# Kernel optimization log

Measured on AMD Instinct MI355X. Metric: run time of the kernel, lower is better.

The kernel has to match this reference:

```python
import jax, jax.numpy as jnp
import numpy as np

B, I, L = 128, 32, 96   # batch, input_dim, time_series_length
H = 512                  # hidden_dim
F = 24                   # forecast_length (t_eval points)
S = 16                   # n_samples


def _lin(k, out_dim, in_dim):
    kw, kb = jax.random.split(k)
    bound = 1.0 / np.sqrt(in_dim)
    W = jax.random.uniform(kw, (out_dim, in_dim), jnp.float32, -bound, bound)
    b = jax.random.uniform(kb, (out_dim,), jnp.float32, -bound, bound)
    return W, b


def setup_inputs() -> dict:
    key = jax.random.key(0)
    ks = jax.random.split(key, 12)
    enc_Wih, enc_bih = _lin(ks[0], 3 * H, I)
    enc_Whh, enc_bhh = _lin(ks[1], 3 * H, H)
    f_W1, f_b1 = _lin(ks[2], H, H)
    f_W2, f_b2 = _lin(ks[3], H, H)
    g_W, g_b = _lin(ks[4], H, H)
    dec_Wih, dec_bih = _lin(ks[5], 3 * H, H)
    dec_Whh, dec_bhh = _lin(ks[6], 3 * H, H)
    out_W, out_b = _lin(ks[7], I, H)
    x = jax.random.normal(ks[8], (B, I, L), jnp.float32)
    noise = jax.random.normal(ks[9], (S, F - 1, B, H), jnp.float32)  # unit normals -> dW = sqrt(dt)*noise
    return dict(x=x, noise=noise,
                enc_Wih=enc_Wih, enc_Whh=enc_Whh, enc_bih=enc_bih, enc_bhh=enc_bhh,
                f_W1=f_W1, f_b1=f_b1, f_W2=f_W2, f_b2=f_b2,
                g_W=g_W, g_b=g_b,
                dec_Wih=dec_Wih, dec_Whh=dec_Whh, dec_bih=dec_bih, dec_bhh=dec_bhh,
                out_W=out_W, out_b=out_b)


def _gru_cell(gi, gh, h):
    ir, iz, inn = jnp.split(gi, 3, axis=-1)
    hr, hz, hn = jnp.split(gh, 3, axis=-1)
    r = jax.nn.sigmoid(ir + hr)
    z = jax.nn.sigmoid(iz + hz)
    n = jnp.tanh(inn + r * hn)
    return (1.0 - z) * n + z * h


def reference(x, noise, enc_Wih, enc_Whh, enc_bih, enc_bhh,
              f_W1, f_b1, f_W2, f_b2, g_W, g_b,
              dec_Wih, dec_Whh, dec_bih, dec_bhh, out_W, out_b):
    Bb, Ii = x.shape[0], x.shape[1]
    Ss, steps = noise.shape[0], noise.shape[1]
    Hh = enc_Whh.shape[1]
    Ff = steps + 1  # forecast_length; t_eval=linspace(0,F,F) -> F-1 euler steps

    # ---- encoder GRU over [B, L, I] (x permuted from [B, I, L]) ----
    xs = jnp.transpose(x, (0, 2, 1))  # [B, L, I]
    gi_all = jnp.einsum('bli,gi->lbg', xs, enc_Wih) + enc_bih  # [L, B, 3H]

    def enc_step(h, gi):
        gh = h @ enc_Whh.T + enc_bhh
        return _gru_cell(gi, gh, h), None

    h0 = jnp.zeros((Bb, Hh), x.dtype)
    h_enc, _ = jax.lax.scan(enc_step, h0, gi_all)  # [B, H]

    # ---- Euler-Maruyama SDE integration, samples merged into batch ----
    dt = Ff / steps  # linspace(0, F, F): dt = F/(F-1)
    sqdt = jnp.sqrt(jnp.asarray(dt, x.dtype))
    h_sde = jnp.broadcast_to(h_enc, (Ss, Bb, Hh)).reshape(Ss * Bb, Hh)
    dW = (noise * sqdt).transpose(1, 0, 2, 3).reshape(steps, Ss * Bb, Hh)

    def sde_step(h, dw):
        f = jnp.tanh(h @ f_W1.T + f_b1) @ f_W2.T + f_b2
        g = jax.nn.softplus(h @ g_W.T + g_b)
        return h + f * dt + g * dw, None

    h_T, _ = jax.lax.scan(sde_step, h_sde, dW)  # [S*B, H]

    # ---- decoder GRU with zero inputs (input proj reduces to bias) ----
    gi0 = dec_bih  # W_ih @ 0 + b_ih

    def dec_step(h, _):
        gh = h @ dec_Whh.T + dec_bhh
        h_new = _gru_cell(gi0, gh, h)
        return h_new, h_new

    _, hs = jax.lax.scan(dec_step, h_T, None, length=Ff)  # [F, S*B, H]

    out = hs @ out_W.T + out_b          # [F, S*B, I]
    out = out.transpose(1, 2, 0)        # [S*B, I, F]
    return out.reshape(Ss, Bb, Ii, Ff)  # [S, B, I, F]
```

## Files before the change

### kernel.cpp

```cpp
#include <hip/hip_runtime.h>
#include <math.h>

typedef __bf16 bf16x8 __attribute__((ext_vector_type(8)));
typedef float f32x4 __attribute__((ext_vector_type(4)));
typedef unsigned long long u64;

#define HD 512
#define NB 128
#define NI 32
#define NL 96
#define NS 16
#define NF 24
#define NSTEP 23
#define PAD 520

#define MFMA16(a,b,c) __builtin_amdgcn_mfma_f32_16x16x32_bf16(a,b,c,0,0,0)

__device__ __forceinline__ unsigned short f2bf(float f) {
    union { float f; unsigned u; } v; v.f = f;
    unsigned r = v.u + 0x7fffu + ((v.u >> 16) & 1u);
    return (unsigned short)(r >> 16);
}
__device__ __forceinline__ float bf2f(unsigned short h) {
    union { unsigned u; float f; } v; v.u = ((unsigned)h) << 16;
    return v.f;
}
__device__ __forceinline__ void split_bf(float v, unsigned short& hi, unsigned short& lo) {
    unsigned short h = f2bf(v);
    hi = h;
    lo = f2bf(v - bf2f(h));
}
__device__ __forceinline__ float sigm(float x) { return 1.0f / (1.0f + __expf(-x)); }
__device__ __forceinline__ float softp(float x) {
    return fmaxf(x, 0.0f) + log1pf(__expf(-fabsf(x)));
}
__device__ __forceinline__ bf16x8 ld8(const unsigned short* p) {
    return *reinterpret_cast<const bf16x8*>(p);
}
__device__ __forceinline__ f32x4 mfma3(bf16x8 ahi, bf16x8 alo, const unsigned short* bp, f32x4 c) {
    bf16x8 bhi = ld8(bp);
    bf16x8 blo = ld8(bp + 8);
    c = MFMA16(ahi, bhi, c);
    c = MFMA16(alo, bhi, c);
    c = MFMA16(ahi, blo, c);
    return c;
}

__global__ void pack_w(const float* __restrict__ W, unsigned short* __restrict__ Wp,
                       int N, int K) {
    int idx = blockIdx.x * 256 + threadIdx.x;
    int total = (N / 16) * (K / 32) * 64;
    if (idx >= total) return;
    int lane = idx & 63;
    int t2 = idx >> 6;
    int KT = K / 32;
    int kt = t2 % KT, nt = t2 / KT;
    const float* src = W + (size_t)(nt * 16 + (lane & 15)) * K + kt * 32 + (lane >> 4) * 8;
    unsigned short* dst = Wp + (size_t)idx * 16;
    #pragma unroll
    for (int j = 0; j < 8; ++j) split_bf(src[j], dst[j], dst[8 + j]);
}

__global__ void pack_x(const float* __restrict__ x, unsigned short* __restrict__ xhi,
                       unsigned short* __restrict__ xlo) {
    int idx = blockIdx.x * 256 + threadIdx.x;
    if (idx >= NL * NB) return;
    int b = idx % NB, l = idx / NB;
    size_t base = (size_t)(l * NB + b) * NI;
    #pragma unroll
    for (int i = 0; i < NI; ++i)
        split_bf(x[((size_t)b * NI + i) * NL + l], xhi[base + i], xlo[base + i]);
}

__global__ __launch_bounds__(512, 2) void coop_all(
    const unsigned short* __restrict__ xhi, const unsigned short* __restrict__ xlo,
    const unsigned short* __restrict__ wih_p, const unsigned short* __restrict__ whh_p,
    const unsigned short* __restrict__ w1_p, const unsigned short* __restrict__ w2_p,
    const unsigned short* __restrict__ gw_p, const unsigned short* __restrict__ dwhh_p,
    const unsigned short* __restrict__ outw_p,
    const float* __restrict__ ebih, const float* __restrict__ ebhh,
    const float* __restrict__ fb1, const float* __restrict__ fb2,
    const float* __restrict__ gb, const float* __restrict__ dbih,
    const float* __restrict__ dbhh, const float* __restrict__ outb,
    const float* __restrict__ noise,
    u64* hS0h, u64* hS0l, u64* hS1h, u64* hS1l,
    float* out, unsigned* bar)
{
    const int bid = blockIdx.x;
    const int tid = threadIdx.x, lane = tid & 63, wv = tid >> 6;
    const int l15 = lane & 15, g4 = lane >> 4;
    const f32x4 zz = {0.f, 0.f, 0.f, 0.f};

    __shared__ float pred[4][8][16][16];
    __shared__ __align__(16) unsigned short hAhi[16][PAD];
    __shared__ __align__(16) unsigned short hAlo[16][PAD];
    __shared__ __align__(16) unsigned short uAhi[16][PAD];
    __shared__ __align__(16) unsigned short uAlo[16][PAD];
    __shared__ __align__(16) unsigned short Shi[16][16], Slo[16][16];

    u64* bufh[2] = {hS0h, hS1h};
    u64* bufl[2] = {hS0l, hS1l};

    {
        const int m = bid >> 5, n = bid & 31;
        unsigned* fl = bar + m * 32;
        float cr = 0.f, cz = 0.f, binx = 0.f, bhnn = 0.f, hcell = 0.f;
        const int crow = tid >> 4, cunit = tid & 15;
        if (tid < 256) {
            int u = n * 16 + cunit;
            cr = ebih[u] + ebhh[u];
            cz = ebih[HD + u] + ebhh[HD + u];
            binx = ebih[2 * HD + u];
            bhnn = ebhh[2 * HD + u];
        }
        #pragma unroll 1
        for (int l = 0; l < NL; ++l) {
            bf16x8 axh, axl;
            if (wv == 0) {
                size_t xb = ((size_t)l * NB + m * 16 + l15) * NI + g4 * 8;
                axh = ld8(xhi + xb);
                axl = ld8(xlo + xb);
            }
            if (l > 0) {
                if (wv == 0) {
                    for (;;) {
                        unsigned v = __hip_atomic_load(fl + (lane & 31),
                                     __ATOMIC_RELAXED, __HIP_MEMORY_SCOPE_AGENT);
                        if (__all((int)(v >= (unsigned)l))) break;
                        __builtin_amdgcn_s_sleep(2);
                    }
                }
                __syncthreads();
            }
            {
                const u64* sh = bufh[l & 1];
                const u64* sl = bufl[l & 1];
                u64 qh[4], ql[4];
                #pragma unroll
                for (int rep = 0; rep < 4; ++rep) {
                    int idx = rep * 512 + tid;
                    int r = idx >> 7, c4 = idx & 127;
                    qh[rep] = __hip_atomic_load(sh + (size_t)(m * 16 + r) * 128 + c4,
                                                __ATOMIC_RELAXED, __HIP_MEMORY_SCOPE_AGENT);
                    ql[rep] = __hip_atomic_load(sl + (size_t)(m * 16 + r) * 128 + c4,
                                                __ATOMIC_RELAXED, __HIP_MEMORY_SCOPE_AGENT);
                }
                #pragma unroll
                for (int rep = 0; rep < 4; ++rep) {
                    int idx = rep * 512 + tid;
                    int r = idx >> 7, c4 = idx & 127;
                    *(u64*)&hAhi[r][c4 * 4] = qh[rep];
                    *(u64*)&hAlo[r][c4 * 4] = ql[rep];
                }
            }
            __syncthreads();
            f32x4 pr = zz, pz = zz, pnh = zz, pnx = zz;
            if (wv == 0) {
                pr  = mfma3(axh, axl, wih_p + ((size_t)(0 * 32 + n) * 64 + lane) * 16, pr);
                pz  = mfma3(axh, axl, wih_p + ((size_t)(1 * 32 + n) * 64 + lane) * 16, pz);
                pnx = mfma3(axh, axl, wih_p + ((size_t)(2 * 32 + n) * 64 + lane) * 16, pnx);
            }
            #pragma unroll
            for (int kk = 0; kk < 2; ++kk) {
                int kt = wv * 2 + kk;
                bf16x8 ah = *(const bf16x8*)&hAhi[l15][kt * 32 + g4 * 8];
                bf16x8 al = *(const bf16x8*)&hAlo[l15][kt * 32 + g4 * 8];
                pr  = mfma3(ah, al, whh_p + ((size_t)((0 * 32 + n) * 16 + kt) * 64 + lane) * 16, pr);
                pz  = mfma3(ah, al, whh_p + ((size_t)((1 * 32 + n) * 16 + kt) * 64 + lane) * 16, pz);
                pnh = mfma3(ah, al, whh_p + ((size_t)((2 * 32 + n) * 16 + kt) * 64 + lane) * 16, pnh);
            }
            #pragma unroll
            for (int v = 0; v < 4; ++v) {
                pred[0][wv][g4 * 4 + v][l15] = pr[v];
                pred[1][wv][g4 * 4 + v][l15] = pz[v];
                pred[2][wv][g4 * 4 + v][l15] = pnh[v];
                if (wv == 0) pred[3][0][g4 * 4 + v][l15] = pnx[v];
            }
            __syncthreads();
            if (tid < 256) {
                float ar = 0.f, az = 0.f, anh_ = 0.f;
                #pragma unroll
                for (int w = 0; w < 8; ++w) {
                    ar += pred[0][w][crow][cunit];
                    az += pred[1][w][crow][cunit];
                    anh_ += pred[2][w][crow][cunit];
                }
                float anx_ = pred[3][0][crow][cunit];
                float r = sigm(ar + cr);
                float z = sigm(az + cz);
                float nn = tanhf(anx_ + binx + r * (anh_ + bhnn));
                hcell = (1.f - z) * nn + z * hcell;
                unsigned short hi, lo;
                split_bf(hcell, hi, lo);
                Shi[crow][cunit] = hi;
                Slo[crow][cunit] = lo;
            }
            __syncthreads();
            if (tid < 128) {
                int p = tid >> 6, t = tid & 63;
                int r = t >> 2, c4 = t & 3;
                u64 q = p ? *(const u64*)&Slo[r][c4 * 4] : *(const u64*)&Shi[r][c4 * 4];
                u64* dst = p ? bufl[(l + 1) & 1] : bufh[(l + 1) & 1];
                __hip_atomic_store(dst + (size_t)(m * 16 + r) * 128 + n * 4 + c4, q,
                                   __ATOMIC_RELAXED, __HIP_MEMORY_SCOPE_AGENT);
            }
            __builtin_amdgcn_s_waitcnt(0);
            __syncthreads();
            if (tid == 0)
                __hip_atomic_store(fl + n, (unsigned)(l + 1),
                                   __ATOMIC_RELAXED, __HIP_MEMORY_SCOPE_AGENT);
        }
        if (tid == 0)
            __hip_atomic_fetch_add(bar + 256, 1u, __ATOMIC_RELAXED, __HIP_MEMORY_SCOPE_AGENT);
    }

    if (bid >= 128) return;

    if (tid == 0) {
        while (__hip_atomic_load(bar + 256, __ATOMIC_RELAXED, __HIP_MEMORY_SCOPE_AGENT) < 256u)
            __builtin_amdgcn_s_sleep(2);
    }
    __syncthreads();

    const int s = bid >> 3, t7 = bid & 7;
    const int brow = t7 * 16;

    for (int i = tid; i < 2048; i += 512) {
        int r = i >> 7, c4 = i & 127;
        u64 qh = __hip_atomic_load(hS0h + (size_t)(brow + r) * 128 + c4, __ATOMIC_RELAXED, __HIP_MEMORY_SCOPE_AGENT);
        u64 ql = __hip_atomic_load(hS0l + (size_t)(brow + r) * 128 + c4, __ATOMIC_RELAXED, __HIP_MEMORY_SCOPE_AGENT);
        *(u64*)&hAhi[r][c4 * 4] = qh;
        *(u64*)&hAlo[r][c4 * 4] = ql;
    }
    __syncthreads();

    float hreg[4][4];
    #pragma unroll
    for (int nt = 0; nt < 4; ++nt)
        #pragma unroll
        for (int v = 0; v < 4; ++v) {
            int u = wv * 64 + nt * 16 + l15;
            hreg[nt][v] = bf2f(hAhi[g4 * 4 + v][u]) + bf2f(hAlo[g4 * 4 + v][u]);
        }

    float b1v[4], b2v[4], gbv[4];
    #pragma unroll
    for (int nt = 0; nt < 4; ++nt) {
        int u = wv * 64 + nt * 16 + l15;
        b1v[nt] = fb1[u]; b2v[nt] = fb2[u]; gbv[nt] = gb[u];
    }
    const float dt = (float)NF / (float)NSTEP;
    const float sqdt = sqrtf(dt);

    #pragma unroll 1
    for (int st = 0; st < NSTEP; ++st) {
        f32x4 au[4], ag[4];
        #pragma unroll
        for (int nt = 0; nt < 4; ++nt) { au[nt] = zz; ag[nt] = zz; }
        #pragma unroll 2
        for (int kt = 0; kt < 16; ++kt) {
            bf16x8 ah = *(const bf16x8*)&hAhi[l15][kt * 32 + g4 * 8];
            bf16x8 al = *(const bf16x8*)&hAlo[l15][kt * 32 + g4 * 8];
            #pragma unroll
            for (int nt = 0; nt < 4; ++nt) {
                int un = wv * 4 + nt;
                au[nt] = mfma3(ah, al, w1_p + ((size_t)(un * 16 + kt) * 64 + lane) * 16, au[nt]);
                ag[nt] = mfma3(ah, al, gw_p + ((size_t)(un * 16 + kt) * 64 + lane) * 16, ag[nt]);
            }
        }
        float nz[4][4];
        #pragma unroll
        for (int nt = 0; nt < 4; ++nt)
            #pragma unroll
            for (int v = 0; v < 4; ++v)
                nz[nt][v] = noise[((size_t)(s * NSTEP + st) * NB + brow + g4 * 4 + v) * HD
                                  + wv * 64 + nt * 16 + l15];
        #pragma unroll
        for (int nt = 0; nt < 4; ++nt)
            #pragma unroll
            for (int v = 0; v < 4; ++v) {
                unsigned short hi, lo;
                split_bf(tanhf(au[nt][v] + b1v[nt]), hi, lo);
                uAhi[g4 * 4 + v][wv * 64 + nt * 16 + l15] = hi;
                uAlo[g4 * 4 + v][wv * 64 + nt * 16 + l15] = lo;
            }
        __syncthreads();
        f32x4 af[4];
        #pragma unroll
        for (int nt = 0; nt < 4; ++nt) af[nt] = zz;
        #pragma unroll 2
        for (int kt = 0; kt < 16; ++kt) {
            bf16x8 uh = *(const bf16x8*)&uAhi[l15][kt * 32 + g4 * 8];
            bf16x8 ul = *(const bf16x8*)&uAlo[l15][kt * 32 + g4 * 8];
            #pragma unroll
            for (int nt = 0; nt < 4; ++nt)
                af[nt] = mfma3(uh, ul, w2_p + ((size_t)((wv * 4 + nt) * 16 + kt) * 64 + lane) * 16, af[nt]);
        }
        #pragma unroll
        for (int nt = 0; nt < 4; ++nt)
            #pragma unroll
            for (int v = 0; v < 4; ++v) {
                float gg = softp(ag[nt][v] + gbv[nt]);
                hreg[nt][v] += (af[nt][v] + b2v[nt]) * dt + gg * sqdt * nz[nt][v];
                unsigned short hi, lo;
                split_bf(hreg[nt][v], hi, lo);
                hAhi[g4 * 4 + v][wv * 64 + nt * 16 + l15] = hi;
                hAlo[g4 * 4 + v][wv * 64 + nt * 16 + l15] = lo;
            }
        __syncthreads();
    }

    float crv[4], czv[4], binv[4], bhnv[4];
    #pragma unroll
    for (int nt = 0; nt < 4; ++nt) {
        int u = wv * 64 + nt * 16 + l15;
        crv[nt] = dbih[u] + dbhh[u];
        czv[nt] = dbih[HD + u] + dbhh[HD + u];
        binv[nt] = dbih[2 * HD + u];
        bhnv[nt] = dbhh[2 * HD + u];
    }
    const float obias = (wv < 2) ? outb[wv * 16 + l15] : 0.f;

    #pragma unroll 1
    for (int j = 0; j <= NF; ++j) {
        if (j >= 1 && wv < 2) {
            f32x4 ao = zz;
            #pragma unroll 2
            for (int kt = 0; kt < 16; ++kt) {
                bf16x8 ah = *(const bf16x8*)&hAhi[l15][kt * 32 + g4 * 8];
                bf16x8 al = *(const bf16x8*)&hAlo[l15][kt * 32 + g4 * 8];
                ao = mfma3(ah, al, outw_p + ((size_t)(wv * 16 + kt) * 64 + lane) * 16, ao);
            }
            #pragma unroll
            for (int v = 0; v < 4; ++v)
                out[(((size_t)s * NB + brow + g4 * 4 + v) * NI + wv * 16 + l15) * NF + (j - 1)]
                    = ao[v] + obias;
        }
        if (j == NF) break;
        f32x4 ar[4], az[4], anh[4];
        #pragma unroll
        for (int nt = 0; nt < 4; ++nt) { ar[nt] = zz; az[nt] = zz; anh[nt] = zz; }
        #pragma unroll 2
        for (int kt = 0; kt < 16; ++kt) {
            bf16x8 ah = *(const bf16x8*)&hAhi[l15][kt * 32 + g4 * 8];
            bf16x8 al = *(const bf16x8*)&hAlo[l15][kt * 32 + g4 * 8];
            #pragma unroll
            for (int nt = 0; nt < 4; ++nt) {
                int un = wv * 4 + nt;
                ar[nt]  = mfma3(ah, al, dwhh_p + ((size_t)((un) * 16 + kt) * 64 + lane) * 16, ar[nt]);
                az[nt]  = mfma3(ah, al, dwhh_p + ((size_t)((32 + un) * 16 + kt) * 64 + lane) * 16, az[nt]);
                anh[nt] = mfma3(ah, al, dwhh_p + ((size_t)((64 + un) * 16 + kt) * 64 + lane) * 16, anh[nt]);
            }
        }
        #pragma unroll
        for (int nt = 0; nt < 4; ++nt)
            #pragma unroll
            for (int v = 0; v < 4; ++v) {
                float r = sigm(ar[nt][v] + crv[nt]);
                float z = sigm(az[nt][v] + czv[nt]);
                float nn2 = tanhf(binv[nt] + r * (anh[nt][v] + bhnv[nt]));
                hreg[nt][v] = (1.f - z) * nn2 + z * hreg[nt][v];
            }
        __syncthreads();
        #pragma unroll
        for (int nt = 0; nt < 4; ++nt)
            #pragma unroll
            for (int v = 0; v < 4; ++v) {
                unsigned short hi, lo;
                split_bf(hreg[nt][v], hi, lo);
                hAhi[g4 * 4 + v][wv * 64 + nt * 16 + l15] = hi;
                hAlo[g4 * 4 + v][wv * 64 + nt * 16 + l15] = lo;
            }
        __syncthreads();
    }
}

extern "C" void kernel_launch(void* const* d_in, const int* in_sizes, int n_in,
                              void* d_out, int out_size, void* d_ws, size_t ws_size,
                              hipStream_t stream) {
    const float* x       = (const float*)d_in[0];
    const float* noise   = (const float*)d_in[1];
    const float* enc_Wih = (const float*)d_in[2];
    const float* enc_Whh = (const float*)d_in[3];
    const float* enc_bih = (const float*)d_in[4];
    const float* enc_bhh = (const float*)d_in[5];
    const float* f_W1    = (const float*)d_in[6];
    const float* f_b1    = (const float*)d_in[7];
    const float* f_W2    = (const float*)d_in[8];
    const float* f_b2    = (const float*)d_in[9];
    const float* g_W     = (const float*)d_in[10];
    const float* g_b     = (const float*)d_in[11];
    const float* dec_Whh = (const float*)d_in[13];
    const float* dec_bih = (const float*)d_in[14];
    const float* dec_bhh = (const float*)d_in[15];
    const float* out_W   = (const float*)d_in[16];
    const float* out_b   = (const float*)d_in[17];
    float* out = (float*)d_out;

    char* ws = (char*)d_ws;
    unsigned short* whh_p  = (unsigned short*)(ws + 0);
    unsigned short* wih_p  = (unsigned short*)(ws + 3145728);
    unsigned short* w1_p   = (unsigned short*)(ws + 3342336);
    unsigned short* w2_p   = (unsigned short*)(ws + 4390912);
    unsigned short* gw_p   = (unsigned short*)(ws + 5439488);
    unsigned short* dwhh_p = (unsigned short*)(ws + 6488064);
    unsigned short* outw_p = (unsigned short*)(ws + 9633792);
    unsigned short* xhi    = (unsigned short*)(ws + 9699328);
    unsigned short* xlo    = (unsigned short*)(ws + 10485760);
    u64*            hS0h   = (u64*)(ws + 11272192);
    u64*            hS0l   = (u64*)(ws + 11403264);
    u64*            hS1h   = (u64*)(ws + 11534336);
    u64*            hS1l   = (u64*)(ws + 11665408);
    unsigned*       bar    = (unsigned*)(ws + 11796480);

    hipMemsetAsync(ws + 11272192, 0, 262144, stream);
    hipMemsetAsync(ws + 11796480, 0, 2048, stream);

    pack_w<<<384, 256, 0, stream>>>(enc_Whh, whh_p, 3 * HD, HD);
    pack_w<<<24, 256, 0, stream>>>(enc_Wih, wih_p, 3 * HD, NI);
    pack_w<<<128, 256, 0, stream>>>(f_W1, w1_p, HD, HD);
    pack_w<<<128, 256, 0, stream>>>(f_W2, w2_p, HD, HD);
    pack_w<<<128, 256, 0, stream>>>(g_W, gw_p, HD, HD);
    pack_w<<<384, 256, 0, stream>>>(dec_Whh, dwhh_p, 3 * HD, HD);
    pack_w<<<8, 256, 0, stream>>>(out_W, outw_p, NI, HD);
    pack_x<<<48, 256, 0, stream>>>(x, xhi, xlo);

    void* args[] = {
        (void*)&xhi, (void*)&xlo, (void*)&wih_p, (void*)&whh_p,
        (void*)&w1_p, (void*)&w2_p, (void*)&gw_p, (void*)&dwhh_p, (void*)&outw_p,
        (void*)&enc_bih, (void*)&enc_bhh, (void*)&f_b1, (void*)&f_b2,
        (void*)&g_b, (void*)&dec_bih, (void*)&dec_bhh, (void*)&out_b,
        (void*)&noise,
        (void*)&hS0h, (void*)&hS0l, (void*)&hS1h, (void*)&hS1l,
        (void*)&out, (void*)&bar
    };
    hipLaunchCooperativeKernel((void*)coop_all, dim3(256), dim3(512), args, 0, stream);
}
```

Baseline: 1.982 ms.

## Split SDE and decoder phases across all 256 blocks with group flag sync

Before, only 128 blocks ran the SDE and decoder phases, each owning 16 rows and all 512 hidden units. Now all 256 blocks take part: groups of 8 blocks share 64 rows, and each block computes a 64-unit column slice. Intermediate activations are exchanged through global buffers with per-group flag barriers. This doubles the active compute units and cuts per-block weight traffic, at the cost of two extra global exchange and sync rounds per SDE step and one per decoder step.

```diff
diff --git a/kernel.cpp b/kernel.cpp
--- a/kernel.cpp
+++ b/kernel.cpp
@@ -44,6 +44,58 @@
     c = MFMA16(alo, bhi, c);
     c = MFMA16(ahi, blo, c);
     return c;
+}
+
+__device__ __forceinline__ void sigval(unsigned* slot, unsigned val, int tid) {
+    __builtin_amdgcn_s_waitcnt(0);
+    __syncthreads();
+    if (tid == 0)
+        __hip_atomic_store(slot, val, __ATOMIC_RELAXED, __HIP_MEMORY_SCOPE_AGENT);
+}
+__device__ __forceinline__ void poll8(const unsigned* f, unsigned tgt, int wv, int lane) {
+    if (wv == 0) {
+        for (;;) {
+            unsigned v = __hip_atomic_load(f + (lane & 7), __ATOMIC_RELAXED, __HIP_MEMORY_SCOPE_AGENT);
+            if (__all((int)(v >= tgt))) break;
+            __builtin_amdgcn_s_sleep(2);
+        }
+    }
+    __syncthreads();
+}
+__device__ __forceinline__ void stage64(const u64* sh, const u64* sl, int r0,
+        unsigned short (*Ahi)[16][PAD], unsigned short (*Alo)[16][PAD], int tid) {
+    #pragma unroll 1
+    for (int c = 0; c < 4; ++c) {
+        u64 th[4], tl[4];
+        #pragma unroll
+        for (int k = 0; k < 4; ++k) {
+            int idx = (c * 4 + k) * 512 + tid;
+            int r = idx >> 7, c4 = idx & 127;
+            th[k] = __hip_atomic_load(sh + (size_t)(r0 + r) * 128 + c4,
+                                      __ATOMIC_RELAXED, __HIP_MEMORY_SCOPE_AGENT);
+            tl[k] = __hip_atomic_load(sl + (size_t)(r0 + r) * 128 + c4,
+                                      __ATOMIC_RELAXED, __HIP_MEMORY_SCOPE_AGENT);
+        }
+        #pragma unroll
+        for (int k = 0; k < 4; ++k) {
+            int idx = (c * 4 + k) * 512 + tid;
+            int r = idx >> 7, c4 = idx & 127;
+            *(u64*)&Ahi[r >> 4][r & 15][c4 * 4] = th[k];
+            *(u64*)&Alo[r >> 4][r & 15][c4 * 4] = tl[k];
+        }
+    }
+}
+__device__ __forceinline__ void publish64(u64* dh, u64* dl, int r0, int u0c,
+        unsigned short (*Bhi)[72], unsigned short (*Blo)[72], int tid) {
+    #pragma unroll
+    for (int rep = 0; rep < 4; ++rep) {
+        int idx = rep * 512 + tid;
+        int pl = idx >> 10, e = idx & 1023;
+        int r = e >> 4, c = e & 15;
+        u64 q = pl ? *(const u64*)&Blo[r][c * 4] : *(const u64*)&Bhi[r][c * 4];
+        u64* dst = (pl ? dl : dh) + (size_t)(r0 + r) * 128 + u0c + c;
+        __hip_atomic_store(dst, q, __ATOMIC_RELAXED, __HIP_MEMORY_SCOPE_AGENT);
+    }
 }
 
 __global__ void pack_w(const float* __restrict__ W, unsigned short* __restrict__ Wp,
@@ -84,6 +136,7 @@
     const float* __restrict__ dbhh, const float* __restrict__ outb,
     const float* __restrict__ noise,
     u64* hS0h, u64* hS0l, u64* hS1h, u64* hS1l,
+    u64* uPh, u64* uPl, u64* hD0h, u64* hD0l, u64* hD1h, u64* hD1l,
     float* out, unsigned* bar)
 {
     const int bid = blockIdx.x;
@@ -91,12 +144,16 @@
     const int l15 = lane & 15, g4 = lane >> 4;
     const f32x4 zz = {0.f, 0.f, 0.f, 0.f};
 
-    __shared__ float pred[4][8][16][16];
-    __shared__ __align__(16) unsigned short hAhi[16][PAD];
-    __shared__ __align__(16) unsigned short hAlo[16][PAD];
-    __shared__ __align__(16) unsigned short uAhi[16][PAD];
-    __shared__ __align__(16) unsigned short uAlo[16][PAD];
-    __shared__ __align__(16) unsigned short Shi[16][16], Slo[16][16];
+    __shared__ __align__(16) unsigned char SM[151552];
+    auto hA64hi = reinterpret_cast<unsigned short (*)[16][PAD]>(SM);
+    auto hA64lo = reinterpret_cast<unsigned short (*)[16][PAD]>(SM + 66560);
+    auto uShi   = reinterpret_cast<unsigned short (*)[72]>(SM + 133120);
+    auto uSlo   = reinterpret_cast<unsigned short (*)[72]>(SM + 142336);
+    auto pred   = reinterpret_cast<float (*)[8][16][16]>(SM);
+    auto ehAhi  = reinterpret_cast<unsigned short (*)[PAD]>(SM + 32768);
+    auto ehAlo  = reinterpret_cast<unsigned short (*)[PAD]>(SM + 49408);
+    auto Shi    = reinterpret_cast<unsigned short (*)[16]>(SM + 66048);
+    auto Slo    = reinterpret_cast<unsigned short (*)[16]>(SM + 66560);
 
     u64* bufh[2] = {hS0h, hS1h};
     u64* bufl[2] = {hS0l, hS1l};
@@ -149,8 +206,8 @@
                 for (int rep = 0; rep < 4; ++rep) {
                     int idx = rep * 512 + tid;
                     int r = idx >> 7, c4 = idx & 127;
-                    *(u64*)&hAhi[r][c4 * 4] = qh[rep];
-                    *(u64*)&hAlo[r][c4 * 4] = ql[rep];
+                    *(u64*)&ehAhi[r][c4 * 4] = qh[rep];
+                    *(u64*)&ehAlo[r][c4 * 4] = ql[rep];
                 }
             }
             __syncthreads();
@@ -163,8 +220,8 @@
             #pragma unroll
             for (int kk = 0; kk < 2; ++kk) {
                 int kt = wv * 2 + kk;
-                bf16x8 ah = *(const bf16x8*)&hAhi[l15][kt * 32 + g4 * 8];
-                bf16x8 al = *(const bf16x8*)&hAlo[l15][kt * 32 + g4 * 8];
+                bf16x8 ah = *(const bf16x8*)&ehAhi[l15][kt * 32 + g4 * 8];
+                bf16x8 al = *(const bf16x8*)&ehAlo[l15][kt * 32 + g4 * 8];
                 pr  = mfma3(ah, al, whh_p + ((size_t)((0 * 32 + n) * 16 + kt) * 64 + lane) * 16, pr);
                 pz  = mfma3(ah, al, whh_p + ((size_t)((1 * 32 + n) * 16 + kt) * 64 + lane) * 16, pz);
                 pnh = mfma3(ah, al, whh_p + ((size_t)((2 * 32 + n) * 16 + kt) * 64 + lane) * 16, pnh);
@@ -214,39 +271,38 @@
             __hip_atomic_fetch_add(bar + 256, 1u, __ATOMIC_RELAXED, __HIP_MEMORY_SCOPE_AGENT);
     }
 
-    if (bid >= 128) return;
-
     if (tid == 0) {
         while (__hip_atomic_load(bar + 256, __ATOMIC_RELAXED, __HIP_MEMORY_SCOPE_AGENT) < 256u)
             __builtin_amdgcn_s_sleep(2);
     }
     __syncthreads();
 
-    const int s = bid >> 3, t7 = bid & 7;
-    const int brow = t7 * 16;
-
-    for (int i = tid; i < 2048; i += 512) {
-        int r = i >> 7, c4 = i & 127;
-        u64 qh = __hip_atomic_load(hS0h + (size_t)(brow + r) * 128 + c4, __ATOMIC_RELAXED, __HIP_MEMORY_SCOPE_AGENT);
-        u64 ql = __hip_atomic_load(hS0l + (size_t)(brow + r) * 128 + c4, __ATOMIC_RELAXED, __HIP_MEMORY_SCOPE_AGENT);
-        *(u64*)&hAhi[r][c4 * 4] = qh;
-        *(u64*)&hAlo[r][c4 * 4] = ql;
-    }
+    const int m2 = bid >> 3, n2 = bid & 7;
+    const int rt = wv & 3, nc = wv >> 2;
+    const int r0g = m2 * 64;
+    const int u0 = n2 * 64, u0c = n2 * 16;
+    const int s = m2 >> 1, b0 = (m2 & 1) * 64;
+    unsigned* uf = bar + 320 + m2 * 8;
+    unsigned* hf = bar + 576 + m2 * 8;
+    u64* hDh[2] = {hD0h, hD1h};
+    u64* hDl[2] = {hD0l, hD1l};
+
+    stage64(hS0h, hS0l, b0, hA64hi, hA64lo, tid);
     __syncthreads();
 
-    float hreg[4][4];
+    float hreg[2][4];
     #pragma unroll
-    for (int nt = 0; nt < 4; ++nt)
+    for (int nt = 0; nt < 2; ++nt)
         #pragma unroll
         for (int v = 0; v < 4; ++v) {
-            int u = wv * 64 + nt * 16 + l15;
-            hreg[nt][v] = bf2f(hAhi[g4 * 4 + v][u]) + bf2f(hAlo[g4 * 4 + v][u]);
-        }
-
-    float b1v[4], b2v[4], gbv[4];
+            int cc = u0 + nc * 32 + nt * 16 + l15;
+            hreg[nt][v] = bf2f(hA64hi[rt][g4 * 4 + v][cc]) + bf2f(hA64lo[rt][g4 * 4 + v][cc]);
+        }
+
+    float b1v[2], b2v[2], gbv[2];
     #pragma unroll
-    for (int nt = 0; nt < 4; ++nt) {
-        int u = wv * 64 + nt * 16 + l15;
+    for (int nt = 0; nt < 2; ++nt) {
+        int u = u0 + nc * 32 + nt * 16 + l15;
         b1v[nt] = fb1[u]; b2v[nt] = fb2[u]; gbv[nt] = gb[u];
     }
     const float dt = (float)NF / (float)NSTEP;
@@ -254,123 +310,138 @@
 
     #pragma unroll 1
     for (int st = 0; st < NSTEP; ++st) {
-        f32x4 au[4], ag[4];
-        #pragma unroll
-        for (int nt = 0; nt < 4; ++nt) { au[nt] = zz; ag[nt] = zz; }
+        f32x4 au[2] = {zz, zz}, ag[2] = {zz, zz};
         #pragma unroll 2
         for (int kt = 0; kt < 16; ++kt) {
-            bf16x8 ah = *(const bf16x8*)&hAhi[l15][kt * 32 + g4 * 8];
-            bf16x8 al = *(const bf16x8*)&hAlo[l15][kt * 32 + g4 * 8];
-            #pragma unroll
-            for (int nt = 0; nt < 4; ++nt) {
-                int un = wv * 4 + nt;
-                au[nt] = mfma3(ah, al, w1_p + ((size_t)(un * 16 + kt) * 64 + lane) * 16, au[nt]);
-                ag[nt] = mfma3(ah, al, gw_p + ((size_t)(un * 16 + kt) * 64 + lane) * 16, ag[nt]);
-            }
-        }
-        float nz[4][4];
-        #pragma unroll
-        for (int nt = 0; nt < 4; ++nt)
+            bf16x8 ah = *(const bf16x8*)&hA64hi[rt][l15][kt * 32 + g4 * 8];
+            bf16x8 al = *(const bf16x8*)&hA64lo[rt][l15][kt * 32 + g4 * 8];
+            #pragma unroll
+            for (int nt = 0; nt < 2; ++nt) {
+                int ntg = n2 * 4 + nc * 2 + nt;
+                au[nt] = mfma3(ah, al, w1_p + ((size_t)(ntg * 16 + kt) * 64 + lane) * 16, au[nt]);
+                ag[nt] = mfma3(ah, al, gw_p + ((size_t)(ntg * 16 + kt) * 64 + lane) * 16, ag[nt]);
+            }
+        }
+        float nz[2][4];
+        #pragma unroll
+        for (int nt = 0; nt < 2; ++nt)
             #pragma unroll
             for (int v = 0; v < 4; ++v)
-                nz[nt][v] = noise[((size_t)(s * NSTEP + st) * NB + brow + g4 * 4 + v) * HD
-                                  + wv * 64 + nt * 16 + l15];
-        #pragma unroll
-        for (int nt = 0; nt < 4; ++nt)
+                nz[nt][v] = noise[((size_t)(s * NSTEP + st) * NB + b0 + rt * 16 + g4 * 4 + v) * HD
+                                  + u0 + nc * 32 + nt * 16 + l15];
+        #pragma unroll
+        for (int nt = 0; nt < 2; ++nt)
             #pragma unroll
             for (int v = 0; v < 4; ++v) {
                 unsigned short hi, lo;
                 split_bf(tanhf(au[nt][v] + b1v[nt]), hi, lo);
-                uAhi[g4 * 4 + v][wv * 64 + nt * 16 + l15] = hi;
-                uAlo[g4 * 4 + v][wv * 64 + nt * 16 + l15] = lo;
+                uShi[rt * 16 + g4 * 4 + v][nc * 32 + nt * 16 + l15] = hi;
+                uSlo[rt * 16 + g4 * 4 + v][nc * 32 + nt * 16 + l15] = lo;
             }
         __syncthreads();
-        f32x4 af[4];
-        #pragma unroll
-        for (int nt = 0; nt < 4; ++nt) af[nt] = zz;
+        publish64(uPh, uPl, r0g, u0c, uShi, uSlo, tid);
+        sigval(uf + n2, (unsigned)(st + 1), tid);
+        poll8(uf, (unsigned)(st + 1), wv, lane);
+        stage64(uPh, uPl, r0g, hA64hi, hA64lo, tid);
+        __syncthreads();
+        f32x4 af[2] = {zz, zz};
         #pragma unroll 2
         for (int kt = 0; kt < 16; ++kt) {
-            bf16x8 uh = *(const bf16x8*)&uAhi[l15][kt * 32 + g4 * 8];
-            bf16x8 ul = *(const bf16x8*)&uAlo[l15][kt * 32 + g4 * 8];
-            #pragma unroll
-            for (int nt = 0; nt < 4; ++nt)
-                af[nt] = mfma3(uh, ul, w2_p + ((size_t)((wv * 4 + nt) * 16 + kt) * 64 + lane) * 16, af[nt]);
-        }
-        #pragma unroll
-        for (int nt = 0; nt < 4; ++nt)
+            bf16x8 uh = *(const bf16x8*)&hA64hi[rt][l15][kt * 32 + g4 * 8];
+            bf16x8 ul = *(const bf16x8*)&hA64lo[rt][l15][kt * 32 + g4 * 8];
+            #pragma unroll
+            for (int nt = 0; nt < 2; ++nt) {
+                int ntg = n2 * 4 + nc * 2 + nt;
+                af[nt] = mfma3(uh, ul, w2_p + ((size_t)(ntg * 16 + kt) * 64 + lane) * 16, af[nt]);
+            }
+        }
+        #pragma unroll
+        for (int nt = 0; nt < 2; ++nt)
             #pragma unroll
             for (int v = 0; v < 4; ++v) {
                 float gg = softp(ag[nt][v] + gbv[nt]);
                 hreg[nt][v] += (af[nt][v] + b2v[nt]) * dt + gg * sqdt * nz[nt][v];
                 unsigned short hi, lo;
                 split_bf(hreg[nt][v], hi, lo);
-                hAhi[g4 * 4 + v][wv * 64 + nt * 16 + l15] = hi;
-                hAlo[g4 * 4 + v][wv * 64 + nt * 16 + l15] = lo;
+                uShi[rt * 16 + g4 * 4 + v][nc * 32 + nt * 16 + l15] = hi;
+                uSlo[rt * 16 + g4 * 4 + v][nc * 32 + nt * 16 + l15] = lo;
             }
         __syncthreads();
-    }
-
-    float crv[4], czv[4], binv[4], bhnv[4];
+        publish64(hDh[(st + 1) & 1], hDl[(st + 1) & 1], r0g, u0c, uShi, uSlo, tid);
+        sigval(hf + n2, (unsigned)(st + 1), tid);
+        poll8(hf, (unsigned)(st + 1), wv, lane);
+        stage64(hDh[(st + 1) & 1], hDl[(st + 1) & 1], r0g, hA64hi, hA64lo, tid);
+        __syncthreads();
+    }
+
+    float crv[2], czv[2], binv[2], bhnv[2];
     #pragma unroll
-    for (int nt = 0; nt < 4; ++nt) {
-        int u = wv * 64 + nt * 16 + l15;
+    for (int nt = 0; nt < 2; ++nt) {
+        int u = u0 + nc * 32 + nt * 16 + l15;
         crv[nt] = dbih[u] + dbhh[u];
         czv[nt] = dbih[HD + u] + dbhh[HD + u];
         binv[nt] = dbih[2 * HD + u];
         bhnv[nt] = dbhh[2 * HD + u];
     }
-    const float obias = (wv < 2) ? outb[wv * 16 + l15] : 0.f;
+    float obias[2] = {0.f, 0.f};
+    if (n2 == 0 && wv < 4) {
+        obias[0] = outb[l15];
+        obias[1] = outb[16 + l15];
+    }
 
     #pragma unroll 1
     for (int j = 0; j <= NF; ++j) {
-        if (j >= 1 && wv < 2) {
-            f32x4 ao = zz;
+        if (j >= 1 && n2 == 0 && wv < 4) {
+            f32x4 ao[2] = {zz, zz};
             #pragma unroll 2
             for (int kt = 0; kt < 16; ++kt) {
-                bf16x8 ah = *(const bf16x8*)&hAhi[l15][kt * 32 + g4 * 8];
-                bf16x8 al = *(const bf16x8*)&hAlo[l15][kt * 32 + g4 * 8];
-                ao = mfma3(ah, al, outw_p + ((size_t)(wv * 16 + kt) * 64 + lane) * 16, ao);
-            }
-            #pragma unroll
-            for (int v = 0; v < 4; ++v)
-                out[(((size_t)s * NB + brow + g4 * 4 + v) * NI + wv * 16 + l15) * NF + (j - 1)]
-                    = ao[v] + obias;
+                bf16x8 ah = *(const bf16x8*)&hA64hi[rt][l15][kt * 32 + g4 * 8];
+                bf16x8 al = *(const bf16x8*)&hA64lo[rt][l15][kt * 32 + g4 * 8];
+                #pragma unroll
+                for (int nt = 0; nt < 2; ++nt)
+                    ao[nt] = mfma3(ah, al, outw_p + ((size_t)(nt * 16 + kt) * 64 + lane) * 16, ao[nt]);
+            }
+            #pragma unroll
+            for (int nt = 0; nt < 2; ++nt)
+                #pragma unroll
+                for (int v = 0; v < 4; ++v) {
+                    int b = b0 + rt * 16 + g4 * 4 + v;
+                    out[(((size_t)s * NB + b) * NI + nt * 16 + l15) * NF + (j - 1)]
+                        = ao[nt][v] + obias[nt];
+                }
         }
         if (j == NF) break;
-        f32x4 ar[4], az[4], anh[4];
-        #pragma unroll
-        for (int nt = 0; nt < 4; ++nt) { ar[nt] = zz; az[nt] = zz; anh[nt] = zz; }
+        f32x4 ar[2] = {zz, zz}, az[2] = {zz, zz}, anh[2] = {zz, zz};
         #pragma unroll 2
         for (int kt = 0; kt < 16; ++kt) {
-            bf16x8 ah = *(const bf16x8*)&hAhi[l15][kt * 32 + g4 * 8];
-            bf16x8 al = *(const bf16x8*)&hAlo[l15][kt * 32 + g4 * 8];
-            #pragma unroll
-            for (int nt = 0; nt < 4; ++nt) {
-                int un = wv * 4 + nt;
-                ar[nt]  = mfma3(ah, al, dwhh_p + ((size_t)((un) * 16 + kt) * 64 + lane) * 16, ar[nt]);
-                az[nt]  = mfma3(ah, al, dwhh_p + ((size_t)((32 + un) * 16 + kt) * 64 + lane) * 16, az[nt]);
-                anh[nt] = mfma3(ah, al, dwhh_p + ((size_t)((64 + un) * 16 + kt) * 64 + lane) * 16, anh[nt]);
-            }
-        }
-        #pragma unroll
-        for (int nt = 0; nt < 4; ++nt)
+            bf16x8 ah = *(const bf16x8*)&hA64hi[rt][l15][kt * 32 + g4 * 8];
+            bf16x8 al = *(const bf16x8*)&hA64lo[rt][l15][kt * 32 + g4 * 8];
+            #pragma unroll
+            for (int nt = 0; nt < 2; ++nt) {
+                int ntg = n2 * 4 + nc * 2 + nt;
+                ar[nt]  = mfma3(ah, al, dwhh_p + ((size_t)((ntg) * 16 + kt) * 64 + lane) * 16, ar[nt]);
+                az[nt]  = mfma3(ah, al, dwhh_p + ((size_t)((32 + ntg) * 16 + kt) * 64 + lane) * 16, az[nt]);
+                anh[nt] = mfma3(ah, al, dwhh_p + ((size_t)((64 + ntg) * 16 + kt) * 64 + lane) * 16, anh[nt]);
+            }
+        }
+        #pragma unroll
+        for (int nt = 0; nt < 2; ++nt)
             #pragma unroll
             for (int v = 0; v < 4; ++v) {
                 float r = sigm(ar[nt][v] + crv[nt]);
                 float z = sigm(az[nt][v] + czv[nt]);
                 float nn2 = tanhf(binv[nt] + r * (anh[nt][v] + bhnv[nt]));
                 hreg[nt][v] = (1.f - z) * nn2 + z * hreg[nt][v];
-            }
-        __syncthreads();
-        #pragma unroll
-        for (int nt = 0; nt < 4; ++nt)
-            #pragma unroll
-            for (int v = 0; v < 4; ++v) {
                 unsigned short hi, lo;
                 split_bf(hreg[nt][v], hi, lo);
-                hAhi[g4 * 4 + v][wv * 64 + nt * 16 + l15] = hi;
-                hAlo[g4 * 4 + v][wv * 64 + nt * 16 + l15] = lo;
-            }
+                uShi[rt * 16 + g4 * 4 + v][nc * 32 + nt * 16 + l15] = hi;
+                uSlo[rt * 16 + g4 * 4 + v][nc * 32 + nt * 16 + l15] = lo;
+            }
+        __syncthreads();
+        publish64(hDh[(NSTEP + j + 1) & 1], hDl[(NSTEP + j + 1) & 1], r0g, u0c, uShi, uSlo, tid);
+        sigval(hf + n2, (unsigned)(NSTEP + j + 1), tid);
+        poll8(hf, (unsigned)(NSTEP + j + 1), wv, lane);
+        stage64(hDh[(NSTEP + j + 1) & 1], hDl[(NSTEP + j + 1) & 1], r0g, hA64hi, hA64lo, tid);
         __syncthreads();
     }
 }
@@ -412,9 +483,15 @@
     u64*            hS1h   = (u64*)(ws + 11534336);
     u64*            hS1l   = (u64*)(ws + 11665408);
     unsigned*       bar    = (unsigned*)(ws + 11796480);
+    u64*            uPh    = (u64*)(ws + 11800576);
+    u64*            uPl    = (u64*)(ws + 13897728);
+    u64*            hD0h   = (u64*)(ws + 15994880);
+    u64*            hD0l   = (u64*)(ws + 18092032);
+    u64*            hD1h   = (u64*)(ws + 20189184);
+    u64*            hD1l   = (u64*)(ws + 22286336);
 
     hipMemsetAsync(ws + 11272192, 0, 262144, stream);
-    hipMemsetAsync(ws + 11796480, 0, 2048, stream);
+    hipMemsetAsync(ws + 11796480, 0, 4096, stream);
 
     pack_w<<<384, 256, 0, stream>>>(enc_Whh, whh_p, 3 * HD, HD);
     pack_w<<<24, 256, 0, stream>>>(enc_Wih, wih_p, 3 * HD, NI);
@@ -432,6 +509,7 @@
         (void*)&g_b, (void*)&dec_bih, (void*)&dec_bhh, (void*)&out_b,
         (void*)&noise,
         (void*)&hS0h, (void*)&hS0l, (void*)&hS1h, (void*)&hS1l,
+        (void*)&uPh, (void*)&uPl, (void*)&hD0h, (void*)&hD0l, (void*)&hD1h, (void*)&hD1l,
         (void*)&out, (void*)&bar
     };
     hipLaunchCooperativeKernel((void*)coop_all, dim3(256), dim3(512), args, 0, stream);
```

Result: faster. 1.862 ms (-6.1%).
